# Kernel optimization log

Measured on AMD Instinct MI355X. Metric: run time of the kernel, lower is better.

Reference implementation:

```python
import jax, jax.numpy as jnp
import numpy as np

B = 8192
E = 1024  # embedding_size
P = 512   # projection_size
TEMPERATURE = 0.1
NEG_INF = -9e15
EPS = 1e-8


def setup_inputs() -> dict:
    key = jax.random.key(0)
    kx, kw, kb = jax.random.split(key, 3)
    x = jax.random.normal(kx, (B, 2 * E), dtype=jnp.float32)
    lim = 1.0 / np.sqrt(E)
    # torch nn.Linear default init: uniform(-1/sqrt(in), 1/sqrt(in))
    w = jax.random.uniform(kw, (E, P), jnp.float32, -lim, lim)
    b = jax.random.uniform(kb, (P,), jnp.float32, -lim, lim)
    return {"x": x, "w": w, "b": b}


def reference(x, w, b):
    e = x.shape[1] // 2
    # NOTE: source applies codon_projection to BOTH halves (aminoacid_projection unused)
    z_codon = jax.nn.relu(x[:, :e]) @ w + b          # [B, P]
    z_amino = jax.nn.relu(x[:, e:]) @ w + b          # [B, P]
    z = jnp.concatenate([z_codon, z_amino], axis=1)  # [B, 2P]

    # cosine similarity via normalize + GEMM instead of O(B^2*D) broadcast
    norm = jnp.maximum(jnp.linalg.norm(z, axis=-1, keepdims=True), EPS)
    zn = z / norm
    cos_sim = zn @ zn.T                              # [B, B]

    n = cos_sim.shape[0]
    idx = jnp.arange(n)
    # mask self-similarity BEFORE temperature division (matches source order)
    cos_sim = jnp.where(idx[:, None] == idx[None, :], NEG_INF, cos_sim)
    cos_sim = cos_sim / TEMPERATURE

    # pos_mask = eye rolled by B//2 along dim 0: pos[i] = cos_sim[i, (i - B//2) % B]
    pos = cos_sim[idx, (idx - n // 2) % n]
    nll = -pos + jax.nn.logsumexp(cos_sim, axis=-1)
    return nll.mean()
```

## Files before the change

### kernel.cpp

```cpp
#include <hip/hip_runtime.h>
#include <hip/hip_bf16.h>
#include <stdint.h>


typedef __attribute__((ext_vector_type(4))) float f32x4;
typedef __attribute__((ext_vector_type(4))) int i32x4;
typedef __attribute__((ext_vector_type(8))) int i32x8;

__device__ __forceinline__ unsigned int enc4(float v) {
  unsigned int s = (__float_as_uint(v) >> 28) & 8u;
  float a = fabsf(v);
  unsigned int m;
  if (a < 0.25f) m = 0u;
  else if (a < 0.75f) m = 1u;
  else if (a < 1.25f) m = 2u;
  else if (a < 1.75f) m = 3u;
  else if (a < 2.5f)  m = 4u;
  else if (a < 3.5f)  m = 5u;
  else if (a < 5.0f)  m = 6u;
  else m = 7u;
  return s | m;
}

__global__ __launch_bounds__(256) void wtr_kernel(
    const float* __restrict__ w, unsigned char* __restrict__ wt8,
    float* __restrict__ sumexp, float* __restrict__ out) {
  __shared__ unsigned char lt[64][68];
  int b = blockIdx.x, t = threadIdx.x;
  int gt = b * 256 + t;
  if (gt < 8192) sumexp[gt] = 0.f;
  if (gt == 0) out[0] = 0.f;
  int k0 = (b >> 3) * 64, n0 = (b & 7) * 64;
  int r = t >> 4, c = t & 15;
#pragma unroll
  for (int i = 0; i < 4; ++i) {
    int kl = i * 16 + r;
    float4 v = *(const float4*)&w[(size_t)(k0 + kl) * 512 + n0 + c * 4];
    int q = __builtin_amdgcn_cvt_pk_fp8_f32(v.x * 64.f, v.y * 64.f, 0, false);
    q = __builtin_amdgcn_cvt_pk_fp8_f32(v.z * 64.f, v.w * 64.f, q, true);
    *(int*)&lt[kl][c * 4] = q;
  }
  __syncthreads();
  int nl = t >> 2, ks = t & 3;
  union { unsigned char b8[16]; i32x4 v4; } u;
#pragma unroll
  for (int j = 0; j < 16; ++j) u.b8[j] = lt[ks * 16 + j][nl];
  *(i32x4*)&wt8[(size_t)(n0 + nl) * 1024 + k0 + ks * 16] = u.v4;
}

__global__ __launch_bounds__(512, 2) void gemm1qn_kernel(
    const float* __restrict__ x, const unsigned char* __restrict__ wt8,
    const float* __restrict__ bias, unsigned char* __restrict__ zn4) {
  __shared__ unsigned char smem[147456] __attribute__((aligned(16)));
  int i0 = blockIdx.x * 64;
  int tid = threadIdx.x, L = tid & 63, w = tid >> 6;
  int l4 = L & 15, q = L >> 4;

  int ra = tid >> 3, kq = tid & 7;
  int Sslot = ((ra * 2) ^ ((ra >> 2) & 7)) ^ (kq & 1);
  int Aoff = (kq >> 1) * 2048 + Sslot * 16;
  const float* xq = x + (size_t)(i0 + ra) * 1024 + kq * 16;

  int e1 = tid ^ ((tid >> 3) & 7);
  int rB = e1 >> 1, hB = e1 & 1;
  const unsigned char* srcB1 = wt8 + (size_t)rB * 1024 + hB * 16;
  const unsigned char* srcB2 = wt8 + (size_t)(rB + 256) * 1024 + hB * 16;

  auto stageB = [&](int buf, int k0) {
#pragma unroll
    for (int p = 0; p < 4; ++p) {
      __builtin_amdgcn_global_load_lds(
          (const __attribute__((address_space(1))) void*)(srcB1 + k0 + p * 32),
          (__attribute__((address_space(3))) void*)(smem + 16384 + buf * 65536 + p * 16384 + tid * 16),
          16, 0, 0);
      __builtin_amdgcn_global_load_lds(
          (const __attribute__((address_space(1))) void*)(srcB2 + k0 + p * 32),
          (__attribute__((address_space(3))) void*)(smem + 16384 + buf * 65536 + p * 16384 + 8192 + tid * 16),
          16, 0, 0);
    }
  };

  auto writeA = [&](int buf, const float4* xv) {
    int pk[4];
#pragma unroll
    for (int j = 0; j < 4; ++j) {
      int p = __builtin_amdgcn_cvt_pk_fp8_f32(fmaxf(xv[j].x, 0.f) * 16.f,
                                              fmaxf(xv[j].y, 0.f) * 16.f, 0, false);
      p = __builtin_amdgcn_cvt_pk_fp8_f32(fmaxf(xv[j].z, 0.f) * 16.f,
                                          fmaxf(xv[j].w, 0.f) * 16.f, p, true);
      pk[j] = p;
    }
    *(i32x4*)(smem + buf * 8192 + Aoff) = (i32x4){pk[0], pk[1], pk[2], pk[3]};
  };

  int pAo[4], pBo[4];
#pragma unroll
  for (int mt = 0; mt < 4; ++mt) {
    int r = mt * 16 + l4;
    pAo[mt] = ((r * 2) ^ ((r >> 2) & 7)) * 16;
  }
#pragma unroll
  for (int nt = 0; nt < 4; ++nt) {
    int r = w * 64 + nt * 16 + l4;
    pBo[nt] = ((r * 2) ^ ((r >> 2) & 7)) * 16;
  }

  f32x4 acc[4][4];
#pragma unroll
  for (int a = 0; a < 4; ++a)
#pragma unroll
    for (int bq = 0; bq < 4; ++bq) acc[a][bq] = (f32x4)0.f;

  float4 xv[4];
#pragma unroll
  for (int j = 0; j < 4; ++j) xv[j] = *(const float4*)(xq + j * 4);
  writeA(0, xv);
  stageB(0, 0);
  __syncthreads();

#pragma unroll 1
  for (int s = 0; s < 8; ++s) {
    if (s < 7) {
#pragma unroll
      for (int j = 0; j < 4; ++j)
        xv[j] = *(const float4*)(xq + (s + 1) * 128 + j * 4);
      stageB((s + 1) & 1, (s + 1) * 128);
    }
    const unsigned char* Ab = smem + (s & 1) * 8192 + q * 2048;
    const unsigned char* Bb = smem + 16384 + (s & 1) * 65536 + q * 16384;
    i32x8 afr[4];
#pragma unroll
    for (int mt = 0; mt < 4; ++mt) {
      i32x4 lo = *(const i32x4*)(Ab + pAo[mt]);
      i32x4 hi = *(const i32x4*)(Ab + (pAo[mt] ^ 16));
      afr[mt] = (i32x8){lo.x, lo.y, lo.z, lo.w, hi.x, hi.y, hi.z, hi.w};
    }
#pragma unroll
    for (int nt = 0; nt < 4; ++nt) {
      i32x4 lo = *(const i32x4*)(Bb + pBo[nt]);
      i32x4 hi = *(const i32x4*)(Bb + (pBo[nt] ^ 16));
      i32x8 bfr = (i32x8){lo.x, lo.y, lo.z, lo.w, hi.x, hi.y, hi.z, hi.w};
#pragma unroll
      for (int mt = 0; mt < 4; ++mt)
        acc[mt][nt] = __builtin_amdgcn_mfma_scale_f32_16x16x128_f8f6f4(
            afr[mt], bfr, acc[mt][nt], 0, 0,
            0, 0x7F7F7F7F, 0, 0x7F7F7F7F);
    }
    if (s < 7) writeA((s + 1) & 1, xv);
    __syncthreads();
  }

  const float SC = 1.0f / 1024.0f;
  float bn[4];
#pragma unroll
  for (int nt = 0; nt < 4; ++nt) bn[nt] = bias[w * 64 + nt * 16 + l4];
  float ssp[4][4];
#pragma unroll
  for (int mt = 0; mt < 4; ++mt)
#pragma unroll
    for (int r = 0; r < 4; ++r) ssp[mt][r] = 0.f;
#pragma unroll
  for (int mt = 0; mt < 4; ++mt)
#pragma unroll
    for (int nt = 0; nt < 4; ++nt)
#pragma unroll
      for (int r = 0; r < 4; ++r) {
        float zv = acc[mt][nt][r] * SC + bn[nt];
        acc[mt][nt][r] = zv;
        ssp[mt][r] += zv * zv;
      }
#pragma unroll
  for (int mt = 0; mt < 4; ++mt)
#pragma unroll
    for (int r = 0; r < 4; ++r) {
      float v = ssp[mt][r];
      v += __shfl_xor(v, 1); v += __shfl_xor(v, 2);
      v += __shfl_xor(v, 4); v += __shfl_xor(v, 8);
      ssp[mt][r] = v;
    }
  float* ssbuf = (float*)smem;
  if (l4 == 0) {
#pragma unroll
    for (int mt = 0; mt < 4; ++mt)
#pragma unroll
      for (int r = 0; r < 4; ++r)
        ssbuf[(mt * 16 + q * 4 + r) * 8 + w] = ssp[mt][r];
  }
  __syncthreads();
  float* invbuf = (float*)(smem + 2048);
  if (tid < 32) {
    float tot = 0.f;
#pragma unroll
    for (int j = 0; j < 8; ++j)
      tot += ssbuf[(2 * tid) * 8 + j] + ssbuf[(2 * tid + 1) * 8 + j];
    invbuf[tid] = 32.f / fmaxf(sqrtf(tot), 1e-8f);
  }
  __syncthreads();
#pragma unroll
  for (int mt = 0; mt < 4; ++mt)
#pragma unroll
    for (int r = 0; r < 4; ++r) {
      int zr = mt * 16 + q * 4 + r;
      float inv = invbuf[zr >> 1];
      int zg = i0 + zr;
      size_t base = (size_t)(zg >> 1) * 512 + (size_t)(zg & 1) * 256;
#pragma unroll
      for (int nt = 0; nt < 4; ++nt) {
        unsigned int n = enc4(acc[mt][nt][r] * inv);
        unsigned int hi = (unsigned int)__shfl_xor((int)n, 1);
        if (!(l4 & 1)) {
          int col = w * 64 + nt * 16 + l4;
          zn4[base + (col >> 1)] = (unsigned char)(n | (hi << 4));
        }
      }
    }
}

__global__ __launch_bounds__(256, 3) void gemm2_kernel(
    const unsigned char* __restrict__ zn4,
    float* __restrict__ sumexp, float* __restrict__ pos) {
  __shared__ unsigned char As[8192] __attribute__((aligned(16)));
  __shared__ unsigned char Bs[8192] __attribute__((aligned(16)));
  int g = (blockIdx.x & 7) * 260 + (blockIdx.x >> 3);
  int SI = 0, rem = g;
#pragma unroll 1
  for (SI = 0; SI < 8; ++SI) {
    int rowcnt = 36 + (7 - SI) * 64;
    if (rem < rowcnt) break;
    rem -= rowcnt;
  }
  int bi, bj;
  if (rem < 36) {
    int ti = 0;
    while (rem >= 8 - ti) { rem -= 8 - ti; ++ti; }
    bi = SI * 8 + ti;
    bj = bi + rem;
  } else {
    rem -= 36;
    int SJ = SI + 1 + (rem >> 6);
    int l = rem & 63;
    bi = SI * 8 + (l >> 3);
    bj = SJ * 8 + (l & 7);
  }
  bool diag = (bi == bj);
  int i0 = bi * 128, j0 = bj * 128;

  int tid = threadIdx.x, L = tid & 63, w = tid >> 6;
  int wm = w >> 1, wn = w & 1;
  int l4 = L & 15, q = L >> 4;

  int strow = tid >> 2;
  int sq = (tid & 3) ^ ((tid >> 3) & 3);
  const unsigned char* Ag  = zn4 + (size_t)(i0 + strow) * 512 + sq * 16;
  const unsigned char* Ag2 = Ag + 64 * 512;
  const unsigned char* Bg  = zn4 + (size_t)(j0 + strow) * 512 + sq * 16;
  const unsigned char* Bg2 = Bg + 64 * 512;
  int ldb = (tid & ~63) * 16;

  int pA[4], pB[4];
#pragma unroll
  for (int mt = 0; mt < 4; ++mt) {
    int r = wm * 64 + mt * 16 + l4;
    pA[mt] = r * 64 + ((q ^ ((r >> 1) & 3)) << 4);
  }
#pragma unroll
  for (int nt = 0; nt < 4; ++nt) {
    int r = wn * 64 + nt * 16 + l4;
    pB[nt] = r * 64 + ((q ^ ((r >> 1) & 3)) << 4);
  }

  f32x4 acc[4][4];
#pragma unroll
  for (int a = 0; a < 4; ++a)
#pragma unroll
    for (int bq = 0; bq < 4; ++bq) acc[a][bq] = (f32x4)0.f;

  const unsigned char* Bsrc = diag ? (const unsigned char*)As : (const unsigned char*)Bs;

#pragma unroll 1
  for (int koff = 0; koff < 512; koff += 64) {
    __syncthreads();
    __builtin_amdgcn_global_load_lds(
        (const __attribute__((address_space(1))) void*)(Ag + koff),
        (__attribute__((address_space(3))) void*)(As + ldb), 16, 0, 0);
    __builtin_amdgcn_global_load_lds(
        (const __attribute__((address_space(1))) void*)(Ag2 + koff),
        (__attribute__((address_space(3))) void*)(As + 4096 + ldb), 16, 0, 0);
    if (!diag) {
      __builtin_amdgcn_global_load_lds(
          (const __attribute__((address_space(1))) void*)(Bg + koff),
          (__attribute__((address_space(3))) void*)(Bs + ldb), 16, 0, 0);
      __builtin_amdgcn_global_load_lds(
          (const __attribute__((address_space(1))) void*)(Bg2 + koff),
          (__attribute__((address_space(3))) void*)(Bs + 4096 + ldb), 16, 0, 0);
    }
    __syncthreads();
    i32x4 a4[4];
#pragma unroll
    for (int mt = 0; mt < 4; ++mt) a4[mt] = *(const i32x4*)(As + pA[mt]);
#pragma unroll
    for (int nt = 0; nt < 4; ++nt) {
      i32x4 b4 = *(const i32x4*)(Bsrc + pB[nt]);
      i32x8 bfr = (i32x8){b4.x, b4.y, b4.z, b4.w, b4.x, b4.y, b4.z, b4.w};
#pragma unroll
      for (int mt = 0; mt < 4; ++mt) {
        i32x8 afr = (i32x8){a4[mt].x, a4[mt].y, a4[mt].z, a4[mt].w,
                            a4[mt].x, a4[mt].y, a4[mt].z, a4[mt].w};
        acc[mt][nt] = __builtin_amdgcn_mfma_scale_f32_16x16x128_f8f6f4(
            afr, bfr, acc[mt][nt], 4, 4,
            0, 0x7F7F7F7F, 0, 0x7F7F7F7F);
      }
    }
  }

  const float SC = 10.0f / 1024.0f;
  float rs[4][4];
  float cs[4] = {0.f, 0.f, 0.f, 0.f};
#pragma unroll
  for (int mt = 0; mt < 4; ++mt)
#pragma unroll
    for (int r = 0; r < 4; ++r) rs[mt][r] = 0.f;
  int ib = i0 + wm * 64 + (q << 2);
  int jb = j0 + wn * 64 + l4;
#pragma unroll
  for (int mt = 0; mt < 4; ++mt)
#pragma unroll
    for (int nt = 0; nt < 4; ++nt) {
      int j = jb + nt * 16;
#pragma unroll
      for (int r = 0; r < 4; ++r) {
        int i = ib + mt * 16 + r;
        float s = acc[mt][nt][r] * SC;
        if (j == (i ^ 4096)) { pos[i] = s; pos[j] = s; }
        float e = (i == j) ? 0.f : __expf(s);
        rs[mt][r] += e;
        if (!diag) cs[nt] += e;
      }
    }
#pragma unroll
  for (int mt = 0; mt < 4; ++mt)
#pragma unroll
    for (int r = 0; r < 4; ++r) {
      float v = rs[mt][r];
      v += __shfl_xor(v, 1); v += __shfl_xor(v, 2);
      v += __shfl_xor(v, 4); v += __shfl_xor(v, 8);
      rs[mt][r] = v;
    }
  int sel = l4;
  float myv = rs[0][0];
#pragma unroll
  for (int mt = 0; mt < 4; ++mt)
#pragma unroll
    for (int r = 0; r < 4; ++r)
      if (sel == mt * 4 + r) myv = rs[mt][r];
  int rowi = i0 + wm * 64 + (sel >> 2) * 16 + (q << 2) + (sel & 3);
  atomicAdd(&sumexp[rowi], myv);
  if (!diag) {
#pragma unroll
    for (int nt = 0; nt < 4; ++nt) {
      float v = cs[nt];
      v += __shfl_xor(v, 16); v += __shfl_xor(v, 32);
      if (q == 0) atomicAdd(&sumexp[jb + nt * 16], v);
    }
  }
}

__global__ __launch_bounds__(512) void finalize_kernel(
    const float* __restrict__ sumexp, const float* __restrict__ pos,
    float* __restrict__ out) {
  int t = threadIdx.x;
  int i = blockIdx.x * 512 + t;
  float s = logf(sumexp[i]) - pos[i];
#pragma unroll
  for (int off = 1; off < 64; off <<= 1) s += __shfl_xor(s, off);
  __shared__ float red[8];
  if ((t & 63) == 0) red[t >> 6] = s;
  __syncthreads();
  if (t == 0) {
    float tot = 0.f;
    for (int k2 = 0; k2 < 8; ++k2) tot += red[k2];
    atomicAdd(out, tot * (1.0f / 8192.0f));
  }
}

extern "C" void kernel_launch(void* const* d_in, const int* in_sizes, int n_in,
                              void* d_out, int out_size, void* d_ws, size_t ws_size,
                              hipStream_t stream) {
  const float* x = (const float*)d_in[0];
  const float* w = (const float*)d_in[1];
  const float* b = (const float*)d_in[2];
  float* out = (float*)d_out;
  char* ws = (char*)d_ws;
  unsigned char* wt8 = (unsigned char*)(ws);
  unsigned char* zn4 = (unsigned char*)(ws + 68157440);
  float* sumexp      = (float*)(ws + 84934656);
  float* pos         = (float*)(ws + 84967424);

  wtr_kernel<<<128, 256, 0, stream>>>(w, wt8, sumexp, out);
  gemm1qn_kernel<<<256, 512, 0, stream>>>(x, wt8, b, zn4);
  gemm2_kernel<<<2080, 256, 0, stream>>>(zn4, sumexp, pos);
  finalize_kernel<<<16, 512, 0, stream>>>(sumexp, pos, out);
}
```

Baseline: 156.5 us.

## Load B fragments directly from global into registers instead of LDS staging

The first GEMM now skips staging the fp8 weight tile in shared memory. Each lane reads its B fragments straight from global memory into double-buffered registers, and the k-loop is fully unrolled to alternate between the two buffers. This shrinks LDS from 144KB to 16KB and drops the min-blocks launch bound, removing the LDS round trip for B. The cost is more register pressure and per-wave global loads that may be less coalesced, since each wave reads its own rows of W.

```diff
diff --git a/kernel.cpp b/kernel.cpp
--- a/kernel.cpp
+++ b/kernel.cpp
@@ -48,37 +48,17 @@
   *(i32x4*)&wt8[(size_t)(n0 + nl) * 1024 + k0 + ks * 16] = u.v4;
 }
 
-__global__ __launch_bounds__(512, 2) void gemm1qn_kernel(
+__global__ __launch_bounds__(512) void gemm1qn_kernel(
     const float* __restrict__ x, const unsigned char* __restrict__ wt8,
     const float* __restrict__ bias, unsigned char* __restrict__ zn4) {
-  __shared__ unsigned char smem[147456] __attribute__((aligned(16)));
+  __shared__ unsigned char smem[16384] __attribute__((aligned(16)));
   int i0 = blockIdx.x * 64;
   int tid = threadIdx.x, L = tid & 63, w = tid >> 6;
   int l4 = L & 15, q = L >> 4;
 
   int ra = tid >> 3, kq = tid & 7;
-  int Sslot = ((ra * 2) ^ ((ra >> 2) & 7)) ^ (kq & 1);
-  int Aoff = (kq >> 1) * 2048 + Sslot * 16;
+  int Aoff = (kq >> 1) * 2048 + ((((ra * 2) ^ ((ra >> 2) & 7)) ^ (kq & 1))) * 16;
   const float* xq = x + (size_t)(i0 + ra) * 1024 + kq * 16;
-
-  int e1 = tid ^ ((tid >> 3) & 7);
-  int rB = e1 >> 1, hB = e1 & 1;
-  const unsigned char* srcB1 = wt8 + (size_t)rB * 1024 + hB * 16;
-  const unsigned char* srcB2 = wt8 + (size_t)(rB + 256) * 1024 + hB * 16;
-
-  auto stageB = [&](int buf, int k0) {
-#pragma unroll
-    for (int p = 0; p < 4; ++p) {
-      __builtin_amdgcn_global_load_lds(
-          (const __attribute__((address_space(1))) void*)(srcB1 + k0 + p * 32),
-          (__attribute__((address_space(3))) void*)(smem + 16384 + buf * 65536 + p * 16384 + tid * 16),
-          16, 0, 0);
-      __builtin_amdgcn_global_load_lds(
-          (const __attribute__((address_space(1))) void*)(srcB2 + k0 + p * 32),
-          (__attribute__((address_space(3))) void*)(smem + 16384 + buf * 65536 + p * 16384 + 8192 + tid * 16),
-          16, 0, 0);
-    }
-  };
 
   auto writeA = [&](int buf, const float4* xv) {
     int pk[4];
@@ -93,16 +73,18 @@
     *(i32x4*)(smem + buf * 8192 + Aoff) = (i32x4){pk[0], pk[1], pk[2], pk[3]};
   };
 
-  int pAo[4], pBo[4];
+  int pAo[4];
 #pragma unroll
   for (int mt = 0; mt < 4; ++mt) {
     int r = mt * 16 + l4;
     pAo[mt] = ((r * 2) ^ ((r >> 2) & 7)) * 16;
   }
+
+  const unsigned char* bp[4];
 #pragma unroll
   for (int nt = 0; nt < 4; ++nt) {
     int r = w * 64 + nt * 16 + l4;
-    pBo[nt] = ((r * 2) ^ ((r >> 2) & 7)) * 16;
+    bp[nt] = wt8 + (size_t)r * 1024 + q * 32;
   }
 
   f32x4 acc[4][4];
@@ -115,19 +97,26 @@
 #pragma unroll
   for (int j = 0; j < 4; ++j) xv[j] = *(const float4*)(xq + j * 4);
   writeA(0, xv);
-  stageB(0, 0);
-  __syncthreads();
-
-#pragma unroll 1
-  for (int s = 0; s < 8; ++s) {
+  i32x4 b0[4][2], b1[4][2];
+#pragma unroll
+  for (int nt = 0; nt < 4; ++nt) {
+    b0[nt][0] = *(const i32x4*)(bp[nt]);
+    b0[nt][1] = *(const i32x4*)(bp[nt] + 16);
+  }
+  __syncthreads();
+
+  auto step = [&](int s, i32x4 (&bu)[4][2], i32x4 (&bl)[4][2]) {
     if (s < 7) {
 #pragma unroll
       for (int j = 0; j < 4; ++j)
         xv[j] = *(const float4*)(xq + (s + 1) * 128 + j * 4);
-      stageB((s + 1) & 1, (s + 1) * 128);
+#pragma unroll
+      for (int nt = 0; nt < 4; ++nt) {
+        bl[nt][0] = *(const i32x4*)(bp[nt] + (s + 1) * 128);
+        bl[nt][1] = *(const i32x4*)(bp[nt] + (s + 1) * 128 + 16);
+      }
     }
     const unsigned char* Ab = smem + (s & 1) * 8192 + q * 2048;
-    const unsigned char* Bb = smem + 16384 + (s & 1) * 65536 + q * 16384;
     i32x8 afr[4];
 #pragma unroll
     for (int mt = 0; mt < 4; ++mt) {
@@ -137,9 +126,8 @@
     }
 #pragma unroll
     for (int nt = 0; nt < 4; ++nt) {
-      i32x4 lo = *(const i32x4*)(Bb + pBo[nt]);
-      i32x4 hi = *(const i32x4*)(Bb + (pBo[nt] ^ 16));
-      i32x8 bfr = (i32x8){lo.x, lo.y, lo.z, lo.w, hi.x, hi.y, hi.z, hi.w};
+      i32x8 bfr = (i32x8){bu[nt][0].x, bu[nt][0].y, bu[nt][0].z, bu[nt][0].w,
+                          bu[nt][1].x, bu[nt][1].y, bu[nt][1].z, bu[nt][1].w};
 #pragma unroll
       for (int mt = 0; mt < 4; ++mt)
         acc[mt][nt] = __builtin_amdgcn_mfma_scale_f32_16x16x128_f8f6f4(
@@ -148,7 +136,9 @@
     }
     if (s < 7) writeA((s + 1) & 1, xv);
     __syncthreads();
-  }
+  };
+  step(0, b0, b1); step(1, b1, b0); step(2, b0, b1); step(3, b1, b0);
+  step(4, b0, b1); step(5, b1, b0); step(6, b0, b1); step(7, b1, b0);
 
   const float SC = 1.0f / 1024.0f;
   float bn[4];
```

Measured after the change: 153.4 us, median of 2. 1.02x faster.
